# Kernel optimization log

Hardware: AMD Instinct MI355X
Metric: run time of the kernel (lower is better)

## Reference

```python
import jax, jax.numpy as jnp
import numpy as np

N, E, F_IN, H, C = 50000, 800000, 128, 4, 73
HC = H * C  # 292
NEG_SLOPE_ATT = 0.2   # GATv2 attention leaky relu
NEG_SLOPE_ACT = 0.01  # F.leaky_relu default
BN_EPS = 1e-5


def setup_inputs() -> dict:
    key = jax.random.key(0)
    ks = jax.random.split(key, 20)
    rn = lambda k, shp, s=0.05: (jax.random.normal(k, shp, jnp.float32) * s)
    inp = {
        'x': jax.random.normal(ks[0], (N, F_IN), jnp.float32),
        'edge_index': jax.random.randint(ks[1], (2, E), 0, N, jnp.int64),
        # conv1 (in=F_IN)
        'Wl1': rn(ks[2], (HC, F_IN)), 'bl1': rn(ks[3], (HC,)),
        'Wr1': rn(ks[4], (HC, F_IN)), 'br1': rn(ks[5], (HC,)),
        'att1': rn(ks[6], (H, C)), 'b1': rn(ks[7], (HC,)),
        # conv2 (in=HC)
        'Wl2': rn(ks[8], (HC, HC)), 'bl2': rn(ks[9], (HC,)),
        'Wr2': rn(ks[10], (HC, HC)), 'br2': rn(ks[11], (HC,)),
        'att2': rn(ks[12], (H, C)), 'b2': rn(ks[13], (HC,)),
        # shared BatchNorm1d(HC)
        'gamma': jnp.ones((HC,), jnp.float32), 'beta': jnp.zeros((HC,), jnp.float32),
        # classifier Linear(HC, 2)
        'Wc': rn(ks[14], (2, HC)), 'bc': rn(ks[15], (2,)),
    }
    return inp


def _gatv2(x, src, dst, Wl, bl, Wr, br, att, b):
    # lin_l on source, lin_r on target (PyG GATv2Conv, share_weights=False)
    xl = (x @ Wl.T + bl).reshape(-1, H, C)  # [N,H,C]
    xr = (x @ Wr.T + br).reshape(-1, H, C)
    f = xl[src] + xr[dst]                    # [E,H,C] edge-wise gather
    s = jnp.einsum('ehc,hc->eh', jax.nn.leaky_relu(f, NEG_SLOPE_ATT), att)
    # segment softmax over incoming edges of each destination node
    m = jax.ops.segment_max(s, dst, num_segments=N)
    ex = jnp.exp(s - m[dst])
    den = jax.ops.segment_sum(ex, dst, num_segments=N)
    alpha = ex / (den[dst] + 1e-16)          # [E,H]
    out = jax.ops.segment_sum(alpha[:, :, None] * xl[src], dst, num_segments=N)
    return out.reshape(-1, HC) + b           # concat heads + bias


def _bn(x, gamma, beta):
    mu = jnp.mean(x, axis=0)
    var = jnp.mean((x - mu) ** 2, axis=0)
    return (x - mu) * jax.lax.rsqrt(var + BN_EPS) * gamma + beta


def reference(x, edge_index, Wl1, bl1, Wr1, br1, att1, b1,
              Wl2, bl2, Wr2, br2, att2, b2, gamma, beta, Wc, bc):
    src, dst = edge_index[0], edge_index[1]
    h = _gatv2(x, src, dst, Wl1, bl1, Wr1, br1, att1, b1)
    h = jax.nn.leaky_relu(_bn(h, gamma, beta), NEG_SLOPE_ACT)
    h = _gatv2(h, src, dst, Wl2, bl2, Wr2, br2, att2, b2)
    h = jax.nn.leaky_relu(_bn(h, gamma, beta), NEG_SLOPE_ACT)
    return h @ Wc.T + bc
```

## Files before the change

### kernel.cpp

```cpp
#include <hip/hip_runtime.h>

#define HCDIM 292
#define NHEAD 4
#define CDIM 73
#define SLOTS 5
#define NPERM 320
#define BN_EPS 1e-5f
#define LOG2E 1.44269504f

using u16x8 = __attribute__((ext_vector_type(8))) unsigned short;
using f32x4 = __attribute__((ext_vector_type(4))) float;
using u16x4 = __attribute__((ext_vector_type(4))) unsigned short;
using hf2   = __attribute__((ext_vector_type(2))) _Float16;
using v2h   = __attribute__((ext_vector_type(2))) __fp16;
using v8h   = __attribute__((ext_vector_type(8))) __fp16;

__device__ inline v2h pkrtz(float a, float b) {
  return __builtin_amdgcn_cvt_pkrtz(a, b);
}
__device__ inline float fdot2(hf2 a, hf2 b, float c) {
  return __builtin_amdgcn_fdot2(__builtin_bit_cast(v2h, a),
                                __builtin_bit_cast(v2h, b), c, false);
}
__device__ inline ushort f2h(float f) {
  _Float16 h = (_Float16)f;
  return __builtin_bit_cast(ushort, h);
}
__device__ inline float h2f(ushort v) {
  return (float)__builtin_bit_cast(_Float16, v);
}
__device__ inline hf2 habs2(hf2 a) {
  unsigned u = __builtin_bit_cast(unsigned, a) & 0x7fff7fffu;
  return __builtin_bit_cast(hf2, u);
}
__device__ inline float fexp2(float x) {
  float r;
  asm("v_exp_f32 %0, %1" : "=v"(r) : "v"(x));
  return r;
}

#define FMAMIX_LO(ACC, W, U)                                                  \
  asm("v_fma_mix_f32 %0, %1, %2, %0 op_sel_hi:[1,0,0]"                        \
      : "+v"(ACC) : "v"(U), "v"(W))
#define FMAMIX_HI(ACC, W, U)                                                  \
  asm("v_fma_mix_f32 %0, %1, %2, %0 op_sel:[1,0,0] op_sel_hi:[1,0,0]"         \
      : "+v"(ACC) : "v"(U), "v"(W))

__device__ inline float dpp16_allsum(float v) {
  union { float f; int i; } a, b;
  a.f = v;
  b.i = __builtin_amdgcn_update_dpp(0, a.i, 0xB1, 0xf, 0xf, true);
  a.f += b.f;
  b.i = __builtin_amdgcn_update_dpp(0, a.i, 0x4E, 0xf, 0xf, true);
  a.f += b.f;
  b.i = __builtin_amdgcn_update_dpp(0, a.i, 0x124, 0xf, 0xf, true);
  a.f += b.f;
  b.i = __builtin_amdgcn_update_dpp(0, a.i, 0x128, 0xf, 0xf, true);
  a.f += b.f;
  return a.f;
}

__device__ inline int perm2feat(int p, bool& valid) {
  int h, c;
  if (p < 256) {
    h = p >> 6;
    c = ((p & 3) << 4) | ((p >> 2) & 15);
    valid = true;
  } else {
    int q = p - 256;
    h = q >> 4;
    c = 64 + (q & 15);
    valid = (q & 15) < (CDIM - 64);
  }
  return h * CDIM + c;
}

__global__ __launch_bounds__(320) void k_prep(
    const float* __restrict__ Wl1, const float* __restrict__ bl1,
    const float* __restrict__ Wr1, const float* __restrict__ br1,
    const float* __restrict__ Wl2, const float* __restrict__ bl2,
    const float* __restrict__ Wr2, const float* __restrict__ br2,
    ushort* __restrict__ wb1, float* __restrict__ pb1,
    ushort* __restrict__ wb2, float* __restrict__ pb2,
    const float* __restrict__ att1, const float* __restrict__ b1v,
    const float* __restrict__ att2, const float* __restrict__ b2v,
    const float* __restrict__ gamma, const float* __restrict__ beta,
    const float* __restrict__ Wc, float* __restrict__ vecp,
    const int* __restrict__ dst, int* __restrict__ deg, int E) {
  int bx = blockIdx.x, t = threadIdx.x;
  if (bx >= 5 * NPERM) {
    int i = (bx - 5 * NPERM) * 320 + t;
    int i4 = i * 4;
    if (i4 + 3 < E) {
      int4 d = *(const int4*)(dst + i4);
      atomicAdd(&deg[d.x], 1);
      atomicAdd(&deg[d.y], 1);
      atomicAdd(&deg[d.z], 1);
      atomicAdd(&deg[d.w], 1);
    } else {
      for (int k = i4; k < E; ++k) atomicAdd(&deg[dst[k]], 1);
    }
    return;
  }
  int seg = bx / NPERM;
  int p = bx - seg * NPERM;
  bool pv;
  int gn = perm2feat(p, pv);
  if (seg == 4) {
    if (t < 8) {
      const float* src;
      switch (t) {
        case 0: src = att1; break;
        case 1: src = b1v; break;
        case 2: src = att2; break;
        case 3: src = b2v; break;
        case 4: src = gamma; break;
        case 5: src = beta; break;
        case 6: src = Wc; break;
        default: src = Wc + HCDIM; break;
      }
      vecp[t * NPERM + p] = pv ? src[gn] : 0.f;
    }
    return;
  }
  const float* W;
  const float* b;
  ushort* Wp;
  float* pb;
  int Kin, Kpad, kperm;
  if (seg < 2) {
    Kin = 128; Kpad = 128; kperm = 0;
    W = seg ? Wr1 : Wl1; b = seg ? br1 : bl1;
    Wp = wb1 + (size_t)seg * NPERM * 128; pb = pb1 + seg * NPERM;
  } else {
    Kin = HCDIM; Kpad = NPERM; kperm = 1;
    int s2 = seg - 2;
    W = s2 ? Wr2 : Wl2; b = s2 ? br2 : bl2;
    Wp = wb2 + (size_t)s2 * NPERM * NPERM; pb = pb2 + s2 * NPERM;
  }
  if (t < Kpad) {
    int gk = t;
    bool kv = t < Kin;
    if (kperm) { bool v2; gk = perm2feat(t, v2); kv = v2; }
    ushort v = 0;
    if (pv && kv) v = f2h(W[(size_t)gn * Kin + gk]);
    Wp[(size_t)p * Kpad + t] = v;
  }
  if (t == 0) pb[p] = pv ? b[gn] : 0.f;
}

__global__ __launch_bounds__(256) void k_scan_lb(const int* __restrict__ deg,
                                                 unsigned* __restrict__ st,
                                                 int* __restrict__ row_ptr,
                                                 int* __restrict__ cursor,
                                                 int n, int E) {
  __shared__ int s[256];
  __shared__ int sprefix;
  int bid = blockIdx.x, t = threadIdx.x;
  int i = bid * 256 + t;
  int v = (i < n) ? deg[i] : 0;
  s[t] = v;
  __syncthreads();
  for (int off = 1; off < 256; off <<= 1) {
    int tv = (t >= off) ? s[t - off] : 0;
    __syncthreads();
    s[t] += tv;
    __syncthreads();
  }
  unsigned total = (unsigned)s[255];
  if (t == 0)
    __hip_atomic_store(&st[bid], (1u << 30) | total, __ATOMIC_RELEASE,
                       __HIP_MEMORY_SCOPE_AGENT);
  if (t < 64) {
    unsigned run = 0;
    int base = bid - 1;
    bool done = (bid == 0);
    while (!done) {
      int p = base - t;
      unsigned myv = 0;
      int stat = 2;
      if (p >= 0) {
        unsigned x;
        do {
          x = __hip_atomic_load(&st[p], __ATOMIC_ACQUIRE,
                                __HIP_MEMORY_SCOPE_AGENT);
          if (x == 0u) __builtin_amdgcn_s_sleep(1);
        } while (x == 0u);
        myv = x & 0x3FFFFFFFu;
        stat = (int)(x >> 30);
      }
      unsigned long long m = __ballot(stat == 2);
      unsigned contrib;
      if (m) {
        int fi = __ffsll((long long)m) - 1;
        contrib = (t <= fi) ? myv : 0u;
        done = true;
      } else {
        contrib = myv;
        base -= 64;
      }
#pragma unroll
      for (int off = 32; off > 0; off >>= 1)
        contrib += (unsigned)__shfl_xor((int)contrib, off, 64);
      run += contrib;
    }
    if (t == 0) {
      __hip_atomic_store(&st[bid], (2u << 30) | (run + total), __ATOMIC_RELEASE,
                         __HIP_MEMORY_SCOPE_AGENT);
      sprefix = (int)run;
    }
  }
  __syncthreads();
  int run = sprefix;
  if (i < n) {
    int rp = run + s[t] - v;
    row_ptr[i] = rp;
    cursor[i] = rp;
  }
  if (i == 0) row_ptr[n] = E;
}

template <int KS, int MODE, int FILL, int ROWS>
__global__ __launch_bounds__(256, 3) void k_gemm_a_lds(
    const void* __restrict__ Av, const ushort* __restrict__ Wb,
    const float* __restrict__ pb, const float* __restrict__ bnsum,
    const float* __restrict__ bnsq, const float* __restrict__ gp,
    const float* __restrict__ btp, float invN, ushort* __restrict__ o0,
    ushort* __restrict__ o1, int M,
    const int* __restrict__ srcs, const int* __restrict__ dsts,
    int* __restrict__ cursor, int* __restrict__ csr_src, int E, int gemmb) {
  const int bx = (int)blockIdx.x;
  if (FILL && bx >= 2 * gemmb) {
    int i = (bx - 2 * gemmb) * 256 + (int)threadIdx.x;
    int i4 = i * 4;
    if (i4 + 3 < E) {
      int4 s = *(const int4*)(srcs + i4);
      int4 d = *(const int4*)(dsts + i4);
      csr_src[atomicAdd(&cursor[d.x], 1)] = s.x;
      csr_src[atomicAdd(&cursor[d.y], 1)] = s.y;
      csr_src[atomicAdd(&cursor[d.z], 1)] = s.z;
      csr_src[atomicAdd(&cursor[d.w], 1)] = s.w;
    } else {
      for (int k = i4; k < E; ++k) {
        int pos = atomicAdd(&cursor[dsts[k]], 1);
        csr_src[pos] = srcs[k];
      }
    }
    return;
  }
  constexpr int KSTEPS = KS / 32;
  constexpr int STR = KS + 8;
  constexpr int MI = ROWS / 16;
  __shared__ ushort As[ROWS * STR];
  __shared__ float sScale[MODE ? NPERM : 1];
  __shared__ float sShift[MODE ? NPERM : 1];
  const int tid = threadIdx.x;
  const int y = (bx >= gemmb) ? 1 : 0;
  const int rbase = (y ? bx - gemmb : bx) * ROWS;
  const int wave = tid >> 6, lane = tid & 63;
  const int quad = lane >> 4, lr = lane & 15;
  const int ct = wave;

  if constexpr (MODE == 0) {
    const float* X = (const float*)Av;
    constexpr int NIT = (ROWS * KS / 16) / 256;
    float4 fv[NIT][4];
    int rowv[NIT], sgv[NIT];
#pragma unroll
    for (int k = 0; k < NIT; ++k) {
      int idx = tid + k * 256;
      int row = idx >> 3, sg = idx & 7;
      int gr = rbase + row;
      if (gr >= M) gr = M - 1;
      const float4* p = (const float4*)(X + (size_t)gr * KS + sg * 16);
      fv[k][0] = p[0]; fv[k][1] = p[1]; fv[k][2] = p[2]; fv[k][3] = p[3];
      rowv[k] = row; sgv[k] = sg;
    }
#pragma unroll
    for (int k = 0; k < NIT; ++k) {
      union { v2h h[4]; u16x8 v; } a, b;
      a.h[0] = pkrtz(fv[k][0].x, fv[k][0].y); a.h[1] = pkrtz(fv[k][0].z, fv[k][0].w);
      a.h[2] = pkrtz(fv[k][1].x, fv[k][1].y); a.h[3] = pkrtz(fv[k][1].z, fv[k][1].w);
      b.h[0] = pkrtz(fv[k][2].x, fv[k][2].y); b.h[1] = pkrtz(fv[k][2].z, fv[k][2].w);
      b.h[2] = pkrtz(fv[k][3].x, fv[k][3].y); b.h[3] = pkrtz(fv[k][3].z, fv[k][3].w);
      *(u16x8*)(As + rowv[k] * STR + sgv[k] * 16) = a.v;
      *(u16x8*)(As + rowv[k] * STR + sgv[k] * 16 + 8) = b.v;
    }
  } else {
    const ushort* Hn = (const ushort*)Av;
    constexpr int NIT = (ROWS * KS / 8) / 256;
    u16x8 hv[NIT];
    int rowv[NIT], c8v[NIT];
#pragma unroll
    for (int k = 0; k < NIT; ++k) {
      int idx = tid + k * 256;
      int row = idx / (KS / 8), c8 = idx - row * (KS / 8);
      int gr = rbase + row;
      if (gr >= M) gr = M - 1;
      hv[k] = *(const u16x8*)(Hn + (size_t)gr * KS + c8 * 8);
      rowv[k] = row; c8v[k] = c8;
    }
    for (int c = tid; c < NPERM; c += 256) {
      float mu = bnsum[c] * invN;
      float var = bnsq[c] * invN - mu * mu;
      float sc = rsqrtf(var + BN_EPS) * gp[c];
      sScale[c] = sc;
      sShift[c] = btp[c] - mu * sc;
    }
    __syncthreads();
#pragma unroll
    for (int k = 0; k < NIT; ++k) {
      u16x8 v = hv[k];
      int c = c8v[k] * 8;
      float4 s0 = *(const float4*)(sScale + c);
      float4 s1 = *(const float4*)(sScale + c + 4);
      float4 t0 = *(const float4*)(sShift + c);
      float4 t1 = *(const float4*)(sShift + c + 4);
      float f[8];
      f[0] = fmaf(h2f(v[0]), s0.x, t0.x);
      f[1] = fmaf(h2f(v[1]), s0.y, t0.y);
      f[2] = fmaf(h2f(v[2]), s0.z, t0.z);
      f[3] = fmaf(h2f(v[3]), s0.w, t0.w);
      f[4] = fmaf(h2f(v[4]), s1.x, t1.x);
      f[5] = fmaf(h2f(v[5]), s1.y, t1.y);
      f[6] = fmaf(h2f(v[6]), s1.z, t1.z);
      f[7] = fmaf(h2f(v[7]), s1.w, t1.w);
#pragma unroll
      for (int j = 0; j < 8; ++j) f[j] = (f[j] > 0.f) ? f[j] : 0.01f * f[j];
      union { v2h h4[4]; u16x8 o; } u;
#pragma unroll
      for (int j = 0; j < 4; ++j) u.h4[j] = pkrtz(f[2 * j], f[2 * j + 1]);
      *(u16x8*)(As + rowv[k] * STR + c8v[k] * 8) = u.o;
    }
  }
  __syncthreads();

  const ushort* arow[MI];
#pragma unroll
  for (int i = 0; i < MI; ++i) arow[i] = As + (i * 16 + lr) * STR;

  const ushort* bcol[5];
#pragma unroll
  for (int i = 0; i < 5; ++i)
    bcol[i] = Wb + (size_t)(y * 320 + ct * 80 + i * 16 + lr) * KS;

  f32x4 acc[MI][5] = {};
  v8h bfb[2][5];
#pragma unroll
  for (int i = 0; i < 5; ++i)
    bfb[0][i] = *(const v8h*)(bcol[i] + quad * 8);
#pragma unroll
  for (int s = 0; s < KSTEPS; ++s) {
    if (s + 1 < KSTEPS) {
#pragma unroll
      for (int i = 0; i < 5; ++i)
        bfb[(s + 1) & 1][i] = *(const v8h*)(bcol[i] + (s + 1) * 32 + quad * 8);
    }
    v8h af[MI];
#pragma unroll
    for (int i = 0; i < MI; ++i)
      af[i] = *(const v8h*)(arow[i] + s * 32 + quad * 8);
    __builtin_amdgcn_sched_barrier(0x7);
#pragma unroll
    for (int ni = 0; ni < 5; ++ni)
#pragma unroll
      for (int mi = 0; mi < MI; ++mi)
        acc[mi][ni] = __builtin_amdgcn_mfma_f32_16x16x32_f16(
            bfb[s & 1][ni], af[mi], acc[mi][ni], 0, 0, 0);
  }

  ushort* out = y ? o1 : o0;
  const int colbase = ct * 80;
  float4 pbv[5];
#pragma unroll
  for (int ni = 0; ni < 5; ++ni)
    pbv[ni] = *(const float4*)(pb + y * 320 + ct * 80 + ni * 16 + quad * 4);
#pragma unroll
  for (int mi = 0; mi < MI; ++mi) {
    int gm = rbase + mi * 16 + lr;
    if (gm >= M) continue;
    ushort* orow = out + (size_t)gm * NPERM + colbase + quad * 4;
#pragma unroll
    for (int ni = 0; ni < 5; ++ni) {
      union { v2h h[2]; u16x4 o; } u;
      u.h[0] = pkrtz(acc[mi][ni][0] + pbv[ni].x, acc[mi][ni][1] + pbv[ni].y);
      u.h[1] = pkrtz(acc[mi][ni][2] + pbv[ni].z, acc[mi][ni][3] + pbv[ni].w);
      *(u16x4*)(orow + ni * 16) = u.o;
    }
  }
}

__global__ __launch_bounds__(128) void k_agg(const ushort* __restrict__ xl,
                                             const ushort* __restrict__ xr,
                                             const int* __restrict__ csr_src,
                                             const int* __restrict__ row_ptr,
                                             const float* __restrict__ attp,
                                             const float* __restrict__ bp,
                                             ushort* __restrict__ out, int n) {
  int wave = threadIdx.x >> 6, lane = threadIdx.x & 63;
  int d = blockIdx.x * 2 + wave;
  if (d >= n) return;
  int start = __builtin_amdgcn_readfirstlane(row_ptr[d]);
  int end = __builtin_amdgcn_readfirstlane(row_ptr[d + 1]);

  float4 bp4 = *(const float4*)(bp + lane * 4);
  float bp5 = bp[256 + lane];

  if (start >= end) {
    union { v2h h[2]; u16x4 o; } u;
    u.h[0] = pkrtz(bp4.x, bp4.y);
    u.h[1] = pkrtz(bp4.z, bp4.w);
    *(u16x4*)(out + (size_t)d * NPERM + lane * 4) = u.o;
    out[(size_t)d * NPERM + 256 + lane] = f2h(bp5);
    return;
  }

  const float C = 0.4f * LOG2E;
  float4 at4 = *(const float4*)(attp + lane * 4);
  hf2 av01{(_Float16)(C * at4.x), (_Float16)(C * at4.y)};
  hf2 av23{(_Float16)(C * at4.z), (_Float16)(C * at4.w)};
  hf2 av5{(_Float16)(C * attp[256 + lane]), (_Float16)0.f};

  hf2 xr01, xr23, xr5;
  {
    uint2 rr = *(const uint2*)(xr + (size_t)d * NPERM + lane * 4);
    xr01 = __builtin_bit_cast(hf2, rr.x);
    xr23 = __builtin_bit_cast(hf2, rr.y);
    xr5 = hf2{__builtin_bit_cast(_Float16, xr[(size_t)d * NPERM + 256 + lane]),
              (_Float16)0.f};
  }
  float Tb = fdot2(xr01, av01, fdot2(xr23, av23, fdot2(xr5, av5, 0.f)));
  Tb = dpp16_allsum(Tb);
  float prv = 1.5f * Tb;
  float acc[SLOTS] = {};
  float den = 0.f;
  int dg = end - start;
  int nfull = dg >> 2;
  int rem = dg & 3;

  uint2 s8[4];
  ushort s1[4];
#pragma unroll
  for (int k = 0; k < 4; ++k) {
    int e = start + k;
    if (e > end - 1) e = end - 1;
    int s = __builtin_amdgcn_readfirstlane(csr_src[e]);
    s8[k] = *(const uint2*)(xl + (size_t)s * NPERM + lane * 4);
    s1[k] = xl[(size_t)s * NPERM + 256 + lane];
  }

  for (int g = 0; g < nfull; ++g) {
    int ebase = start + g * 4 + 4;
    uint2 n8[4];
    ushort n1[4];
#pragma unroll
    for (int k = 0; k < 4; ++k) {
      int e = ebase + k;
      if (e > end - 1) e = end - 1;
      int s = __builtin_amdgcn_readfirstlane(csr_src[e]);
      n8[k] = *(const uint2*)(xl + (size_t)s * NPERM + lane * 4);
      n1[k] = xl[(size_t)s * NPERM + 256 + lane];
    }

    float z[4];
#pragma unroll
    for (int k = 0; k < 4; ++k) {
      hf2 x01 = __builtin_bit_cast(hf2, s8[k].x);
      hf2 x23 = __builtin_bit_cast(hf2, s8[k].y);
      hf2 x5{__builtin_bit_cast(_Float16, s1[k]), (_Float16)0.f};
      float T = fdot2(habs2(x01 + xr01), av01,
                fdot2(habs2(x23 + xr23), av23,
                fdot2(habs2(x5 + xr5), av5, 0.f)));
      float Tl = fdot2(x01, av01, fdot2(x23, av23, fdot2(x5, av5, 0.f)));
      z[k] = fmaf(1.5f, Tl, T);
    }
#pragma unroll
    for (int k = 0; k < 4; ++k) z[k] = dpp16_allsum(z[k]);
    float w[4];
#pragma unroll
    for (int k = 0; k < 4; ++k) {
      w[k] = fexp2(fminf(z[k] + prv, 80.f));
      den += w[k];
    }
#pragma unroll
    for (int k = 0; k < 4; ++k) {
      unsigned ux = s8[k].x, uy = s8[k].y, u5 = (unsigned)s1[k];
      FMAMIX_LO(acc[0], w[k], ux);
      FMAMIX_HI(acc[1], w[k], ux);
      FMAMIX_LO(acc[2], w[k], uy);
      FMAMIX_HI(acc[3], w[k], uy);
      FMAMIX_LO(acc[4], w[k], u5);
    }
#pragma unroll
    for (int k = 0; k < 4; ++k) { s8[k] = n8[k]; s1[k] = n1[k]; }
  }

#pragma unroll
  for (int k = 0; k < 3; ++k) {
    if (k < rem) {
      hf2 x01 = __builtin_bit_cast(hf2, s8[k].x);
      hf2 x23 = __builtin_bit_cast(hf2, s8[k].y);
      hf2 x5{__builtin_bit_cast(_Float16, s1[k]), (_Float16)0.f};
      float T = fdot2(habs2(x01 + xr01), av01,
                fdot2(habs2(x23 + xr23), av23,
                fdot2(habs2(x5 + xr5), av5, 0.f)));
      float Tl = fdot2(x01, av01, fdot2(x23, av23, fdot2(x5, av5, 0.f)));
      float z = fmaf(1.5f, Tl, T);
      z = dpp16_allsum(z);
      float w = fexp2(fminf(z + prv, 80.f));
      den += w;
      unsigned ux = s8[k].x, uy = s8[k].y, u5 = (unsigned)s1[k];
      FMAMIX_LO(acc[0], w, ux);
      FMAMIX_HI(acc[1], w, ux);
      FMAMIX_LO(acc[2], w, uy);
      FMAMIX_HI(acc[3], w, uy);
      FMAMIX_LO(acc[4], w, u5);
    }
  }

  float inv = 1.f / (den + 1e-16f);
  union { v2h h[2]; u16x4 o; } u;
  u.h[0] = pkrtz(fmaf(acc[0], inv, bp4.x), fmaf(acc[1], inv, bp4.y));
  u.h[1] = pkrtz(fmaf(acc[2], inv, bp4.z), fmaf(acc[3], inv, bp4.w));
  *(u16x4*)(out + (size_t)d * NPERM + lane * 4) = u.o;
  out[(size_t)d * NPERM + 256 + lane] = f2h(fmaf(acc[4], inv, bp5));
}

__global__ __launch_bounds__(320) void k_bn_reduce(const ushort* __restrict__ h,
                                                   float* __restrict__ colsum,
                                                   float* __restrict__ colsq,
                                                   int n, int rows_per_block) {
  int c = threadIdx.x;
  int r0 = blockIdx.x * rows_per_block;
  int r1 = min(r0 + rows_per_block, n);
  float s = 0.f, s2 = 0.f;
  for (int r = r0; r < r1; ++r) {
    float v = h2f(h[(size_t)r * NPERM + c]);
    s += v;
    s2 += v * v;
  }
  atomicAdd(&colsum[c], s);
  atomicAdd(&colsq[c], s2);
}

__global__ __launch_bounds__(256) void k_bn_classifier(
    const ushort* __restrict__ h, const float* __restrict__ bnsum,
    const float* __restrict__ bnsq, const float* __restrict__ gp,
    const float* __restrict__ btp, float invN, const float* __restrict__ wc0,
    const float* __restrict__ wc1, const float* __restrict__ bc,
    float* __restrict__ out, int n) {
  int wave = threadIdx.x >> 6, lane = threadIdx.x & 63;
  int r = blockIdx.x * 4 + wave;
  if (r >= n) return;
  float a0 = 0.f, a1 = 0.f;
#pragma unroll
  for (int k = 0; k < SLOTS; ++k) {
    int slot = lane + 64 * k;
    float mu = bnsum[slot] * invN;
    float var = bnsq[slot] * invN - mu * mu;
    float sc = rsqrtf(var + BN_EPS) * gp[slot];
    float sh = btp[slot] - mu * sc;
    float v = fmaf(h2f(h[(size_t)r * NPERM + slot]), sc, sh);
    v = (v > 0.f) ? v : 0.01f * v;
    a0 = fmaf(v, wc0[slot], a0);
    a1 = fmaf(v, wc1[slot], a1);
  }
#pragma unroll
  for (int off = 32; off > 0; off >>= 1) {
    a0 += __shfl_xor(a0, off, 64);
    a1 += __shfl_xor(a1, off, 64);
  }
  if (lane == 0) {
    out[(size_t)2 * r] = a0 + bc[0];
    out[(size_t)2 * r + 1] = a1 + bc[1];
  }
}

extern "C" void kernel_launch(void* const* d_in, const int* in_sizes, int n_in,
                              void* d_out, int out_size, void* d_ws, size_t ws_size,
                              hipStream_t stream) {
  const float* x      = (const float*)d_in[0];
  const int*   eidx   = (const int*)d_in[1];
  const float* Wl1    = (const float*)d_in[2];
  const float* bl1    = (const float*)d_in[3];
  const float* Wr1    = (const float*)d_in[4];
  const float* br1    = (const float*)d_in[5];
  const float* att1   = (const float*)d_in[6];
  const float* b1     = (const float*)d_in[7];
  const float* Wl2    = (const float*)d_in[8];
  const float* bl2    = (const float*)d_in[9];
  const float* Wr2    = (const float*)d_in[10];
  const float* br2    = (const float*)d_in[11];
  const float* att2   = (const float*)d_in[12];
  const float* b2     = (const float*)d_in[13];
  const float* gamma  = (const float*)d_in[14];
  const float* beta   = (const float*)d_in[15];
  const float* Wc     = (const float*)d_in[16];
  const float* bc     = (const float*)d_in[17];
  float* out = (float*)d_out;

  const int FIN = 128;
  const int N = in_sizes[0] / FIN;
  const int E = in_sizes[1] / 2;

  const int* src = eidx;
  const int* dst = eidx + E;

  ushort* h      = (ushort*)d_ws;
  ushort* xl     = h + (size_t)N * NPERM;
  ushort* xr     = xl + (size_t)N * NPERM;
  ushort* wb1    = xr + (size_t)N * NPERM;
  ushort* wb2    = wb1 + (size_t)2 * NPERM * 128;
  float* pb1     = (float*)(wb2 + (size_t)2 * NPERM * NPERM);
  float* pb2     = pb1 + 2 * NPERM;
  float* vecp    = pb2 + 2 * NPERM;
  int* row_ptr   = (int*)(vecp + 8 * NPERM);
  int* cursor    = row_ptr + N + 1;
  int* csr_src   = cursor + N;
  int* deg       = csr_src + E;
  unsigned* scanst = (unsigned*)(deg + N);
  int* tickets   = (int*)(scanst + 256);
  float* colsum1 = (float*)(tickets + 4);
  float* colsq1  = colsum1 + NPERM;
  float* colsum2 = colsq1 + NPERM;
  float* colsq2  = colsum2 + NPERM;
  const size_t zero_bytes = (size_t)(N + 256 + 4 + 4 * NPERM) * 4;

  const int G = (N + 255) / 256;
  const int AGGB = (N + 3) / 4;
  const int AGG2 = (N + 1) / 2;
  const int GEMMB = (N + 63) / 64;
  const int FB = (E + 1023) / 1024;
  const int HISTB = (E + 1279) / 1280;

  const float* att1p = vecp;
  const float* b1p   = vecp + NPERM;
  const float* att2p = vecp + 2 * NPERM;
  const float* b2p   = vecp + 3 * NPERM;
  const float* gp    = vecp + 4 * NPERM;
  const float* btp   = vecp + 5 * NPERM;
  const float* wc0   = vecp + 6 * NPERM;
  const float* wc1   = vecp + 7 * NPERM;

  const int BNB = 1024;
  const int RPB = (N + BNB - 1) / BNB;
  const float invN = 1.f / (float)N;

  hipMemsetAsync(deg, 0, zero_bytes, stream);
  k_prep<<<5 * NPERM + HISTB, 320, 0, stream>>>(
      Wl1, bl1, Wr1, br1, Wl2, bl2, Wr2, br2, wb1, pb1, wb2, pb2,
      att1, b1, att2, b2, gamma, beta, Wc, vecp, dst, deg, E);
  k_scan_lb<<<G, 256, 0, stream>>>(deg, scanst, row_ptr, cursor, N, E);
  k_gemm_a_lds<128, 0, 1, 64><<<2 * GEMMB + FB, 256, 0, stream>>>(
      (const void*)x, wb1, pb1, nullptr, nullptr, nullptr, nullptr, 0.f,
      xl, xr, N, src, dst, cursor, csr_src, E, GEMMB);
  k_agg<<<AGG2, 128, 0, stream>>>(xl, xr, csr_src, row_ptr, att1p, b1p, h, N);
  k_bn_reduce<<<BNB, NPERM, 0, stream>>>(h, colsum1, colsq1, N, RPB);
  k_gemm_a_lds<NPERM, 1, 0, 64><<<2 * GEMMB, 256, 0, stream>>>(
      (const void*)h, wb2, pb2, colsum1, colsq1, gp, btp, invN,
      xl, xr, N, nullptr, nullptr, nullptr, nullptr, 0, GEMMB);
  k_agg<<<AGG2, 128, 0, stream>>>(xl, xr, csr_src, row_ptr, att2p, b2p, h, N);
  k_bn_reduce<<<BNB, NPERM, 0, stream>>>(h, colsum2, colsq2, N, RPB);
  k_bn_classifier<<<AGGB, 256, 0, stream>>>(h, colsum2, colsq2, gp, btp, invN,
                                            wc0, wc1, bc, out, N);
}
```

Before: 555.8 us.

## Shard degree/cursor atomics 8-way and compute both projections per GEMM block

Degree histogram and CSR fill now use 8 replicated counter arrays, selected by block index, to spread atomic contention. The scan sums the replicas and writes a per-replica cursor offset. Separately, each GEMM block now computes both the xl and xr projections from a single LDS-staged A tile, halving A loads and BN-transform work. The costs are 8x larger memset and scan reads, a longer serial loop per block with more register pressure, and CSR neighbor order that is no longer the same as before.

```diff
diff --git a/kernel.cpp b/kernel.cpp
--- a/kernel.cpp
+++ b/kernel.cpp
@@ -86,19 +86,21 @@
     const float* __restrict__ att2, const float* __restrict__ b2v,
     const float* __restrict__ gamma, const float* __restrict__ beta,
     const float* __restrict__ Wc, float* __restrict__ vecp,
-    const int* __restrict__ dst, int* __restrict__ deg, int E) {
+    const int* __restrict__ dst, int* __restrict__ deg8, int E, int n) {
   int bx = blockIdx.x, t = threadIdx.x;
   if (bx >= 5 * NPERM) {
-    int i = (bx - 5 * NPERM) * 320 + t;
+    int j = bx - 5 * NPERM;
+    int* dga = deg8 + (size_t)(j & 7) * n;
+    int i = j * 320 + t;
     int i4 = i * 4;
     if (i4 + 3 < E) {
       int4 d = *(const int4*)(dst + i4);
-      atomicAdd(&deg[d.x], 1);
-      atomicAdd(&deg[d.y], 1);
-      atomicAdd(&deg[d.z], 1);
-      atomicAdd(&deg[d.w], 1);
+      atomicAdd(&dga[d.x], 1);
+      atomicAdd(&dga[d.y], 1);
+      atomicAdd(&dga[d.z], 1);
+      atomicAdd(&dga[d.w], 1);
     } else {
-      for (int k = i4; k < E; ++k) atomicAdd(&deg[dst[k]], 1);
+      for (int k = i4; k < E; ++k) atomicAdd(&dga[dst[k]], 1);
     }
     return;
   }
@@ -149,16 +151,22 @@
   if (t == 0) pb[p] = pv ? b[gn] : 0.f;
 }
 
-__global__ __launch_bounds__(256) void k_scan_lb(const int* __restrict__ deg,
+__global__ __launch_bounds__(256) void k_scan_lb(const int* __restrict__ deg8,
                                                  unsigned* __restrict__ st,
                                                  int* __restrict__ row_ptr,
-                                                 int* __restrict__ cursor,
+                                                 int* __restrict__ cursor8,
                                                  int n, int E) {
   __shared__ int s[256];
   __shared__ int sprefix;
   int bid = blockIdx.x, t = threadIdx.x;
   int i = bid * 256 + t;
-  int v = (i < n) ? deg[i] : 0;
+  int dv[8];
+  int v = 0;
+#pragma unroll
+  for (int x = 0; x < 8; ++x) {
+    dv[x] = (i < n) ? deg8[(size_t)x * n + i] : 0;
+    v += dv[x];
+  }
   s[t] = v;
   __syncthreads();
   for (int off = 1; off < 256; off <<= 1) {
@@ -215,7 +223,12 @@
   if (i < n) {
     int rp = run + s[t] - v;
     row_ptr[i] = rp;
-    cursor[i] = rp;
+    int c = rp;
+#pragma unroll
+    for (int x = 0; x < 8; ++x) {
+      cursor8[(size_t)x * n + i] = c;
+      c += dv[x];
+    }
   }
   if (i == 0) row_ptr[n] = E;
 }
@@ -228,22 +241,21 @@
     const float* __restrict__ btp, float invN, ushort* __restrict__ o0,
     ushort* __restrict__ o1, int M,
     const int* __restrict__ srcs, const int* __restrict__ dsts,
-    int* __restrict__ cursor, int* __restrict__ csr_src, int E, int gemmb) {
+    int* __restrict__ cursor8, int* __restrict__ csr_src, int E, int gemmb,
+    int fillb) {
   const int bx = (int)blockIdx.x;
-  if (FILL && bx >= 2 * gemmb) {
-    int i = (bx - 2 * gemmb) * 256 + (int)threadIdx.x;
-    int i4 = i * 4;
-    if (i4 + 3 < E) {
-      int4 s = *(const int4*)(srcs + i4);
-      int4 d = *(const int4*)(dsts + i4);
-      csr_src[atomicAdd(&cursor[d.x], 1)] = s.x;
-      csr_src[atomicAdd(&cursor[d.y], 1)] = s.y;
-      csr_src[atomicAdd(&cursor[d.z], 1)] = s.z;
-      csr_src[atomicAdd(&cursor[d.w], 1)] = s.w;
-    } else {
-      for (int k = i4; k < E; ++k) {
-        int pos = atomicAdd(&cursor[dsts[k]], 1);
-        csr_src[pos] = srcs[k];
+  if (FILL && bx >= gemmb) {
+    if (bx < fillb) return;
+    int f = bx - fillb;
+    int* cur = cursor8 + (size_t)(f & 7) * M;
+    int base = f * 1280 + (int)threadIdx.x * 5;
+#pragma unroll
+    for (int k = 0; k < 5; ++k) {
+      int e = base + k;
+      if (e < E) {
+        int sv = srcs[e];
+        int dv = dsts[e];
+        csr_src[atomicAdd(&cur[dv], 1)] = sv;
       }
     }
     return;
@@ -255,8 +267,7 @@
   __shared__ float sScale[MODE ? NPERM : 1];
   __shared__ float sShift[MODE ? NPERM : 1];
   const int tid = threadIdx.x;
-  const int y = (bx >= gemmb) ? 1 : 0;
-  const int rbase = (y ? bx - gemmb : bx) * ROWS;
+  const int rbase = bx * ROWS;
   const int wave = tid >> 6, lane = tid & 63;
   const int quad = lane >> 4, lr = lane & 15;
   const int ct = wave;
@@ -339,53 +350,56 @@
 #pragma unroll
   for (int i = 0; i < MI; ++i) arow[i] = As + (i * 16 + lr) * STR;
 
-  const ushort* bcol[5];
-#pragma unroll
-  for (int i = 0; i < 5; ++i)
-    bcol[i] = Wb + (size_t)(y * 320 + ct * 80 + i * 16 + lr) * KS;
-
-  f32x4 acc[MI][5] = {};
-  v8h bfb[2][5];
-#pragma unroll
-  for (int i = 0; i < 5; ++i)
-    bfb[0][i] = *(const v8h*)(bcol[i] + quad * 8);
-#pragma unroll
-  for (int s = 0; s < KSTEPS; ++s) {
-    if (s + 1 < KSTEPS) {
-#pragma unroll
-      for (int i = 0; i < 5; ++i)
-        bfb[(s + 1) & 1][i] = *(const v8h*)(bcol[i] + (s + 1) * 32 + quad * 8);
-    }
-    v8h af[MI];
-#pragma unroll
-    for (int i = 0; i < MI; ++i)
-      af[i] = *(const v8h*)(arow[i] + s * 32 + quad * 8);
-    __builtin_amdgcn_sched_barrier(0x7);
+#pragma unroll
+  for (int y = 0; y < 2; ++y) {
+    const ushort* bcol[5];
+#pragma unroll
+    for (int i = 0; i < 5; ++i)
+      bcol[i] = Wb + (size_t)(y * 320 + ct * 80 + i * 16 + lr) * KS;
+
+    f32x4 acc[MI][5] = {};
+    v8h bfb[2][5];
+#pragma unroll
+    for (int i = 0; i < 5; ++i)
+      bfb[0][i] = *(const v8h*)(bcol[i] + quad * 8);
+#pragma unroll
+    for (int s = 0; s < KSTEPS; ++s) {
+      if (s + 1 < KSTEPS) {
+#pragma unroll
+        for (int i = 0; i < 5; ++i)
+          bfb[(s + 1) & 1][i] = *(const v8h*)(bcol[i] + (s + 1) * 32 + quad * 8);
+      }
+      v8h af[MI];
+#pragma unroll
+      for (int i = 0; i < MI; ++i)
+        af[i] = *(const v8h*)(arow[i] + s * 32 + quad * 8);
+      __builtin_amdgcn_sched_barrier(0x7);
+#pragma unroll
+      for (int ni = 0; ni < 5; ++ni)
+#pragma unroll
+        for (int mi = 0; mi < MI; ++mi)
+          acc[mi][ni] = __builtin_amdgcn_mfma_f32_16x16x32_f16(
+              bfb[s & 1][ni], af[mi], acc[mi][ni], 0, 0, 0);
+    }
+
+    ushort* out = y ? o1 : o0;
+    const int colbase = ct * 80;
+    float4 pbv[5];
 #pragma unroll
     for (int ni = 0; ni < 5; ++ni)
-#pragma unroll
-      for (int mi = 0; mi < MI; ++mi)
-        acc[mi][ni] = __builtin_amdgcn_mfma_f32_16x16x32_f16(
-            bfb[s & 1][ni], af[mi], acc[mi][ni], 0, 0, 0);
-  }
-
-  ushort* out = y ? o1 : o0;
-  const int colbase = ct * 80;
-  float4 pbv[5];
-#pragma unroll
-  for (int ni = 0; ni < 5; ++ni)
-    pbv[ni] = *(const float4*)(pb + y * 320 + ct * 80 + ni * 16 + quad * 4);
-#pragma unroll
-  for (int mi = 0; mi < MI; ++mi) {
-    int gm = rbase + mi * 16 + lr;
-    if (gm >= M) continue;
-    ushort* orow = out + (size_t)gm * NPERM + colbase + quad * 4;
-#pragma unroll
-    for (int ni = 0; ni < 5; ++ni) {
-      union { v2h h[2]; u16x4 o; } u;
-      u.h[0] = pkrtz(acc[mi][ni][0] + pbv[ni].x, acc[mi][ni][1] + pbv[ni].y);
-      u.h[1] = pkrtz(acc[mi][ni][2] + pbv[ni].z, acc[mi][ni][3] + pbv[ni].w);
-      *(u16x4*)(orow + ni * 16) = u.o;
+      pbv[ni] = *(const float4*)(pb + y * 320 + ct * 80 + ni * 16 + quad * 4);
+#pragma unroll
+    for (int mi = 0; mi < MI; ++mi) {
+      int gm = rbase + mi * 16 + lr;
+      if (gm >= M) continue;
+      ushort* orow = out + (size_t)gm * NPERM + colbase + quad * 4;
+#pragma unroll
+      for (int ni = 0; ni < 5; ++ni) {
+        union { v2h h[2]; u16x4 o; } u;
+        u.h[0] = pkrtz(acc[mi][ni][0] + pbv[ni].x, acc[mi][ni][1] + pbv[ni].y);
+        u.h[1] = pkrtz(acc[mi][ni][2] + pbv[ni].z, acc[mi][ni][3] + pbv[ni].w);
+        *(u16x4*)(orow + ni * 16) = u.o;
+      }
     }
   }
 }
@@ -615,22 +629,23 @@
   float* pb2     = pb1 + 2 * NPERM;
   float* vecp    = pb2 + 2 * NPERM;
   int* row_ptr   = (int*)(vecp + 8 * NPERM);
-  int* cursor    = row_ptr + N + 1;
-  int* csr_src   = cursor + N;
-  int* deg       = csr_src + E;
-  unsigned* scanst = (unsigned*)(deg + N);
+  int* cursor8   = row_ptr + N + 1;
+  int* csr_src   = cursor8 + 8 * (size_t)N;
+  int* deg8      = csr_src + E;
+  unsigned* scanst = (unsigned*)(deg8 + 8 * (size_t)N);
   int* tickets   = (int*)(scanst + 256);
   float* colsum1 = (float*)(tickets + 4);
   float* colsq1  = colsum1 + NPERM;
   float* colsum2 = colsq1 + NPERM;
   float* colsq2  = colsum2 + NPERM;
-  const size_t zero_bytes = (size_t)(N + 256 + 4 + 4 * NPERM) * 4;
+  const size_t zero_bytes = (size_t)(8 * (size_t)N + 256 + 4 + 4 * NPERM) * 4;
 
   const int G = (N + 255) / 256;
   const int AGGB = (N + 3) / 4;
   const int AGG2 = (N + 1) / 2;
   const int GEMMB = (N + 63) / 64;
-  const int FB = (E + 1023) / 1024;
+  const int FILLB = (GEMMB + 7) & ~7;
+  const int FB = (E + 1279) / 1280;
   const int HISTB = (E + 1279) / 1280;
 
   const float* att1p = vecp;
@@ -646,19 +661,19 @@
   const int RPB = (N + BNB - 1) / BNB;
   const float invN = 1.f / (float)N;
 
-  hipMemsetAsync(deg, 0, zero_bytes, stream);
+  hipMemsetAsync(deg8, 0, zero_bytes, stream);
   k_prep<<<5 * NPERM + HISTB, 320, 0, stream>>>(
       Wl1, bl1, Wr1, br1, Wl2, bl2, Wr2, br2, wb1, pb1, wb2, pb2,
-      att1, b1, att2, b2, gamma, beta, Wc, vecp, dst, deg, E);
-  k_scan_lb<<<G, 256, 0, stream>>>(deg, scanst, row_ptr, cursor, N, E);
-  k_gemm_a_lds<128, 0, 1, 64><<<2 * GEMMB + FB, 256, 0, stream>>>(
+      att1, b1, att2, b2, gamma, beta, Wc, vecp, dst, deg8, E, N);
+  k_scan_lb<<<G, 256, 0, stream>>>(deg8, scanst, row_ptr, cursor8, N, E);
+  k_gemm_a_lds<128, 0, 1, 64><<<FILLB + FB, 256, 0, stream>>>(
       (const void*)x, wb1, pb1, nullptr, nullptr, nullptr, nullptr, 0.f,
-      xl, xr, N, src, dst, cursor, csr_src, E, GEMMB);
+      xl, xr, N, src, dst, cursor8, csr_src, E, GEMMB, FILLB);
   k_agg<<<AGG2, 128, 0, stream>>>(xl, xr, csr_src, row_ptr, att1p, b1p, h, N);
   k_bn_reduce<<<BNB, NPERM, 0, stream>>>(h, colsum1, colsq1, N, RPB);
-  k_gemm_a_lds<NPERM, 1, 0, 64><<<2 * GEMMB, 256, 0, stream>>>(
+  k_gemm_a_lds<NPERM, 1, 0, 64><<<GEMMB, 256, 0, stream>>>(
       (const void*)h, wb2, pb2, colsum1, colsq1, gp, btp, invN,
-      xl, xr, N, nullptr, nullptr, nullptr, nullptr, 0, GEMMB);
+      xl, xr, N, nullptr, nullptr, nullptr, nullptr, 0, GEMMB, GEMMB);
   k_agg<<<AGG2, 128, 0, stream>>>(xl, xr, csr_src, row_ptr, att2p, b2p, h, N);
   k_bn_reduce<<<BNB, NPERM, 0, stream>>>(h, colsum2, colsq2, N, RPB);
   k_bn_classifier<<<AGGB, 256, 0, stream>>>(h, colsum2, colsq2, gp, btp, invN,
```

Measured after the change: 545.0 us. About the same (-1.9%).
